# Kernel tuning notes

Measured on AMD Instinct MI355X. Metric: run time of the kernel, lower is better.

Reference implementation:

```python
import jax, jax.numpy as jnp
import numpy as np
import math

B, S, HID, NH, INTER, L = 8, 512, 768, 12, 3072, 4
DH = HID // NH
EPS = 1e-12


def setup_inputs() -> dict:
    key = jax.random.key(0)
    ks = jax.random.split(key, 12)
    s = 0.02
    hidden_states = jax.random.normal(ks[0], (B, S, HID), jnp.float32)
    lengths = jax.random.randint(ks[1], (B,), S // 2, S + 1)
    attention_mask = (jnp.arange(S)[None, :] < lengths[:, None]).astype(jnp.float32)
    return dict(
        hidden_states=hidden_states,
        attention_mask=attention_mask,
        Wqkv_w=jax.random.normal(ks[2], (L, 3 * HID, HID), jnp.float32) * s,
        Wqkv_b=jnp.zeros((L, 3 * HID), jnp.float32),
        attn_out_w=jax.random.normal(ks[3], (L, HID, HID), jnp.float32) * s,
        attn_out_b=jnp.zeros((L, HID), jnp.float32),
        ln1_g=jnp.ones((L, HID), jnp.float32),
        ln1_b=jnp.zeros((L, HID), jnp.float32),
        glu_w=jax.random.normal(ks[4], (L, 2 * INTER, HID), jnp.float32) * s,
        wo_w=jax.random.normal(ks[5], (L, HID, INTER), jnp.float32) * s,
        wo_b=jnp.zeros((L, HID), jnp.float32),
        ln2_g=jnp.ones((L, HID), jnp.float32),
        ln2_b=jnp.zeros((L, HID), jnp.float32),
        r1=1.0 + 0.1 * jax.random.normal(ks[6], (L, NH, 1, 1), jnp.float32),
        r2=1.0 + 0.1 * jax.random.normal(ks[7], (L, NH, 1, 1), jnp.float32),
        r3=1.0 + 0.1 * jax.random.normal(ks[8], (L, NH, 1, 1), jnp.float32),
    )


def _ln(x, g, b):
    mu = x.mean(-1, keepdims=True)
    var = ((x - mu) ** 2).mean(-1, keepdims=True)
    return (x - mu) / jnp.sqrt(var + EPS) * g + b


def _forward(hidden_states, attention_mask, Wqkv_w, Wqkv_b, attn_out_w, attn_out_b,
             ln1_g, ln1_b, glu_w, wo_w, wo_b, ln2_g, ln2_b, r1, r2, r3):
    mask = attention_mask  # [B,S] float, 1=valid
    pos = jnp.arange(S)
    rel = jnp.abs(pos[None, :] - pos[:, None]).astype(jnp.float32)  # [S,S]
    rel_pos = rel > 0
    attn_bias = (1.0 - mask)[:, None, None, :] * -10000.0  # [B,1,1,S]
    # unpad_input <-> zero invalid rows of padded tensor
    h = hidden_states * mask[:, :, None]
    for l in range(L):
        c1 = jnp.clip(r1[l], 1e-7)  # [NH,1,1]
        c2 = jnp.clip(r2[l], 1e-7)
        c3 = jnp.clip(r3[l], 1e-7)
        relp = jnp.where(rel_pos, rel, 1.0) ** c3  # [NH,S,S], safe pow at |i-j|=0
        relp = jnp.where(rel_pos, relp, 0.0)
        kb = -c1 * jnp.log1p(c2 * relp)  # kerple bias [NH,S,S]
        bias = attn_bias + kb[None]  # [B,NH,S,S]
        # qkv on valid tokens only (pad_input reinserts zeros)
        qkv = (h @ Wqkv_w[l].T + Wqkv_b[l]) * mask[:, :, None]
        qkv = qkv.reshape(B, S, 3, NH, DH)
        q = qkv[:, :, 0].transpose(0, 2, 1, 3)  # [B,NH,S,DH]
        k = qkv[:, :, 1].transpose(0, 2, 1, 3)
        v = qkv[:, :, 2].transpose(0, 2, 1, 3)
        scores = jnp.einsum('bhqd,bhkd->bhqk', q, k) / math.sqrt(DH) + bias
        probs = jax.nn.softmax(scores, axis=-1)
        attn = jnp.einsum('bhqk,bhkd->bhqd', probs, v)
        attn = attn.transpose(0, 2, 1, 3).reshape(B, S, HID)
        ao = _ln(attn @ attn_out_w[l].T + attn_out_b[l] + h, ln1_g[l], ln1_b[l])
        ao = ao * mask[:, :, None]
        g = ao @ glu_w[l].T  # [B,S,2*INTER]
        x = jax.nn.gelu(g[..., :INTER], approximate=False) * g[..., INTER:]
        h = _ln(x @ wo_w[l].T + wo_b[l] + ao, ln2_g[l], ln2_b[l])
        h = h * mask[:, :, None]
    return h


def reference(hidden_states, attention_mask, Wqkv_w, Wqkv_b, attn_out_w, attn_out_b,
              ln1_g, ln1_b, glu_w, wo_w, wo_b, ln2_g, ln2_b, r1, r2, r3):
    return _forward(hidden_states, attention_mask, Wqkv_w, Wqkv_b, attn_out_w,
                    attn_out_b, ln1_g, ln1_b, glu_w, wo_w, wo_b, ln2_g, ln2_b,
                    r1, r2, r3)
```

## Files before the change

### kernel.cpp

```cpp
#include <hip/hip_runtime.h>
#include <hip/hip_bf16.h>
#include <math.h>

#define BQ 8
#define SQ 512
#define HID 768
#define NH 12
#define DH 64
#define INTER 3072
#define NL 4
#define M_TOK (BQ*SQ)

typedef unsigned short ushort_t;
typedef __attribute__((ext_vector_type(8))) short bf16x8;
typedef __attribute__((ext_vector_type(8))) unsigned short u16x8;
typedef __attribute__((ext_vector_type(4))) float f32x4;

__device__ __forceinline__ float bf2f(ushort_t u) {
  union { float f; unsigned int i; } v; v.i = ((unsigned int)u) << 16; return v.f;
}
__device__ __forceinline__ ushort_t f2bf(float f) {
  __hip_bfloat16 h = __float2bfloat16(f);
  return *reinterpret_cast<ushort_t*>(&h);
}

__device__ __forceinline__ void gload_lds16(const ushort_t* g, ushort_t* l) {
  __builtin_amdgcn_global_load_lds(
      (const __attribute__((address_space(1))) void*)g,
      (__attribute__((address_space(3))) void*)l, 16, 0, 0);
}

template<int N>
__device__ __forceinline__ void wait_vm() {
  if constexpr (N == 0)      asm volatile("s_waitcnt vmcnt(0)" ::: "memory");
  else if constexpr (N == 6) asm volatile("s_waitcnt vmcnt(6)" ::: "memory");
  else if constexpr (N == 8) asm volatile("s_waitcnt vmcnt(8)" ::: "memory");
  else                       asm volatile("s_waitcnt vmcnt(12)" ::: "memory");
}

__global__ __launch_bounds__(256) void prep_kernel(
    const float* __restrict__ hidden, const float* __restrict__ amask,
    float* __restrict__ maskf, float* __restrict__ maskbias,
    float* __restrict__ h, ushort_t* __restrict__ hb)
{
  int i = blockIdx.x * 256 + threadIdx.x;
  if (i < M_TOK * HID) {
    float m = amask[i / HID];
    float v = hidden[i] * m;
    h[i] = v;
    hb[i] = f2bf(v);
    if (i < M_TOK) {
      maskf[i] = amask[i];
      maskbias[i] = (1.0f - amask[i]) * (-10000.0f);
    }
  }
}

__global__ void kerple_all_kernel(const float* __restrict__ r1,
                                  const float* __restrict__ r2,
                                  const float* __restrict__ r3,
                                  float* __restrict__ kbt_all)
{
  int lh = blockIdx.x;
  int d  = threadIdx.x;
  float c1 = fmaxf(r1[lh], 1e-7f);
  float c2 = fmaxf(r2[lh], 1e-7f);
  float c3 = fmaxf(r3[lh], 1e-7f);
  float v = 0.0f;
  if (d > 0) v = -c1 * log1pf(c2 * powf((float)d, c3));
  kbt_all[lh * SQ + d] = v;
}

#define WS0 (3*HID*HID)
#define WS1 (HID*HID)
#define WS2 (2*INTER*HID)
#define WS3 (HID*INTER)
#define WTOT (WS0+WS1+WS2+WS3)

__global__ __launch_bounds__(256) void wcast_layer_kernel(
    const float* __restrict__ w0, const float* __restrict__ w1,
    const float* __restrict__ w2, const float* __restrict__ w3,
    ushort_t* __restrict__ dst)
{
  int i = (blockIdx.x * 256 + threadIdx.x) * 4;
  if (i >= WTOT) return;
  const float* src; int off;
  if (i < WS0)                { src = w0; off = i; }
  else if (i < WS0+WS1)       { src = w1; off = i - WS0; }
  else if (i < WS0+WS1+WS2)   { src = w2; off = i - WS0 - WS1; }
  else                        { src = w3; off = i - WS0 - WS1 - WS2; }
  float4 v = *reinterpret_cast<const float4*>(src + off);
  ushort4 o;
  o.x = f2bf(v.x); o.y = f2bf(v.y); o.z = f2bf(v.z); o.w = f2bf(v.w);
  *reinterpret_cast<ushort4*>(dst + i) = o;
}

template<int MF, int NB, int BK, int EPI, int VN, int DB>
__global__ __launch_bounds__(256, 2) void mfma_gemm(
    const ushort_t* __restrict__ A, const ushort_t* __restrict__ B0p,
    const ushort_t* __restrict__ B1p, const float* __restrict__ bias,
    const float* __restrict__ rowscale, ushort_t* __restrict__ Cb,
    int N, int K)
{
  constexpr int BM   = MF * 32;
  constexpr int SMK  = BK / 8 - 1;
  constexpr int SSH  = (BK == 32) ? 1 : 0;
  constexpr int AIS  = (BM * BK * 2) / 4096;
  constexpr int BIS  = (128 * BK * 2) / 4096;
  constexpr int KH   = BK / 32;
  constexpr int NBUF = DB ? 2 : 1;

  __shared__ ushort_t As_[NBUF][BM * BK];
  __shared__ ushort_t Bs_[NBUF][NB][128 * BK];

  int tid = threadIdx.x;
  int lane = tid & 63, w = tid >> 6;
  int wr = w >> 1, wc = w & 1;
  int g = lane >> 4, r = lane & 15;

  int NBn = gridDim.x, NBm = gridDim.y;
  int lin = blockIdx.y * NBn + blockIdx.x;
  int cpx = (NBn * NBm) >> 3;
  int wg2 = (lin & 7) * cpx + (lin >> 3);
  int bn = wg2 / NBm, bm = wg2 % NBm;

  f32x4 acc[NB][MF][4];
#pragma unroll
  for (int p = 0; p < NB; ++p)
#pragma unroll
    for (int m = 0; m < MF; ++m)
#pragma unroll
      for (int n = 0; n < 4; ++n) acc[p][m][n] = (f32x4){0.f, 0.f, 0.f, 0.f};

  const ushort_t* Arow  = A   + (size_t)bm * BM * K;
  const ushort_t* Brow0 = B0p + (size_t)bn * 128 * K;
  const ushort_t* Brow1 = (NB == 2) ? (B1p + (size_t)bn * 128 * K) : nullptr;

  auto stage = [&](const ushort_t* base, ushort_t* lds, int k0, int ISS_w) {
#pragma unroll
    for (int i = 0; i < 4; ++i) {
      if (i >= ISS_w) break;
      int o   = (w * ISS_w + i) * 1024 + lane * 16;
      int row = o / (BK * 2);
      int pc  = (o >> 4) & SMK;
      int lc  = pc ^ ((row >> SSH) & SMK);
      gload_lds16(base + (size_t)row * K + k0 + lc * 8,
                  lds + ((w * ISS_w + i) << 9));
    }
  };
  auto stage_all = [&](int k0, int buf) {
    stage(Arow,  &As_[buf][0],    k0, AIS);
    stage(Brow0, &Bs_[buf][0][0], k0, BIS);
    if constexpr (NB == 2) stage(Brow1, &Bs_[buf][1][0], k0, BIS);
  };
  auto compute = [&](int buf) {
#pragma unroll
    for (int kh = 0; kh < KH; ++kh) {
      bf16x8 af[MF], bf_[4];
#pragma unroll
      for (int m = 0; m < MF; ++m)
        af[m] = *(const bf16x8*)(&As_[buf][(wr * (BM/2) + m * 16 + r) * BK
                  + (((kh * 4 + g) ^ ((r >> SSH) & SMK)) * 8)]);
#pragma unroll
      for (int n = 0; n < 4; ++n)
        bf_[n] = *(const bf16x8*)(&Bs_[buf][0][(wc * 64 + n * 16 + r) * BK
                  + (((kh * 4 + g) ^ ((r >> SSH) & SMK)) * 8)]);
#pragma unroll
      for (int m = 0; m < MF; ++m)
#pragma unroll
        for (int n = 0; n < 4; ++n)
          acc[0][m][n] = __builtin_amdgcn_mfma_f32_16x16x32_bf16(
              af[m], bf_[n], acc[0][m][n], 0, 0, 0);
      if constexpr (NB == 2) {
        bf16x8 bg[4];
#pragma unroll
        for (int n = 0; n < 4; ++n)
          bg[n] = *(const bf16x8*)(&Bs_[buf][1][(wc * 64 + n * 16 + r) * BK
                    + (((kh * 4 + g) ^ ((r >> SSH) & SMK)) * 8)]);
#pragma unroll
        for (int m = 0; m < MF; ++m)
#pragma unroll
          for (int n = 0; n < 4; ++n)
            acc[1][m][n] = __builtin_amdgcn_mfma_f32_16x16x32_bf16(
                af[m], bg[n], acc[1][m][n], 0, 0, 0);
      }
    }
  };

  int NT = K / BK;
  if constexpr (DB) {
    stage_all(0, 0);
    for (int t = 0; t < NT; ++t) {
      int cur = t & 1;
      if (t + 1 < NT) {
        stage_all((t + 1) * BK, cur ^ 1);
        wait_vm<VN>();
      } else {
        wait_vm<0>();
      }
      __builtin_amdgcn_s_barrier();
      compute(cur);
      __builtin_amdgcn_s_barrier();
    }
  } else {
    for (int t = 0; t < NT; ++t) {
      stage_all(t * BK, 0);
      wait_vm<0>();
      __builtin_amdgcn_s_barrier();
      compute(0);
      __builtin_amdgcn_s_barrier();
    }
  }

  int r0 = bm * BM + wr * (BM/2), c0 = bn * 128 + wc * 64;
#pragma unroll
  for (int m = 0; m < MF; ++m)
#pragma unroll
    for (int n = 0; n < 4; ++n) {
      int col  = c0 + n * 16 + (lane & 15);
      int rowb = r0 + m * 16 + (lane >> 4) * 4;
      if constexpr (EPI == 0) {
        float bv = bias ? bias[col] : 0.0f;
#pragma unroll
        for (int j = 0; j < 4; ++j)
          Cb[(size_t)(rowb + j) * N + col] = f2bf(acc[0][m][n][j] + bv);
      } else if constexpr (EPI == 1) {
#pragma unroll
        for (int j = 0; j < 4; ++j) {
          float va = acc[0][m][n][j];
          float vb = acc[1][m][n][j];
          float ge = 0.5f * va * (1.0f + erff(va * 0.70710678118654752440f));
          Cb[(size_t)(rowb + j) * N + col] = f2bf(ge * vb);
        }
      } else {
        float bv = bias ? bias[col] : 0.0f;
#pragma unroll
        for (int j = 0; j < 4; ++j) {
          float v = (acc[0][m][n][j] + bv) * rowscale[rowb + j];
          Cb[(size_t)(rowb + j) * N + col] = f2bf(v);
        }
      }
    }
}

__global__ __launch_bounds__(256) void attn_mfma(
    const ushort_t* __restrict__ qkvb, const float* __restrict__ kbt,
    const float* __restrict__ maskbias, ushort_t* __restrict__ attnb)
{
  __shared__ ushort_t Ks[64 * 64];
  __shared__ ushort_t Vt[64 * 64];
  __shared__ ushort_t Ps[64 * 64];
  __shared__ float    kbs[SQ];
  __shared__ float    mbs[SQ];

  int tid  = threadIdx.x;
  int lane = tid & 63, w = tid >> 6;
  int g = lane >> 4, r = lane & 15;
  int bid = blockIdx.x;
  int qt = (bid >> 3) & 7;
  int t_ = (bid & 7) * 12 + (bid >> 6);
  int hh = t_ % NH;
  int b  = t_ / NH;
  int q0 = qt * 64;

  for (int i = tid; i < SQ; i += 256) {
    kbs[i] = kbt[hh * SQ + i];
    mbs[i] = maskbias[b * SQ + i];
  }

  bf16x8 qf[2];
  {
    const ushort_t* qsrc = qkvb + (size_t)(b * SQ + q0 + w * 16 + r) * (3 * HID)
                         + hh * DH + g * 8;
    qf[0] = *(const bf16x8*)(qsrc);
    qf[1] = *(const bf16x8*)(qsrc + 32);
  }

  float m_run[4], l_run[4];
  f32x4 oacc[4];
#pragma unroll
  for (int j = 0; j < 4; ++j) { m_run[j] = -1e30f; l_run[j] = 0.f; }
#pragma unroll
  for (int nd = 0; nd < 4; ++nd) oacc[nd] = (f32x4){0.f, 0.f, 0.f, 0.f};

  int k2 = (tid & 31) * 2, dg = tid >> 5;

  for (int kc = 0; kc < 8; ++kc) {
    __syncthreads();
#pragma unroll
    for (int ii = 0; ii < 2; ++ii) {
      int row = (w * 2 + ii) * 8 + (lane >> 3);
      int c   = lane & 7;
      const ushort_t* src = qkvb + (size_t)(b * SQ + kc * 64 + row) * (3 * HID)
                          + HID + hh * DH + ((c ^ (row & 7)) * 8);
      gload_lds16(src, Ks + (w * 2 + ii) * 512 + lane * 8);
    }
    {
      const ushort_t* v0 = qkvb + (size_t)(b * SQ + kc * 64 + k2) * (3 * HID)
                         + 2 * HID + hh * DH + dg * 8;
      const ushort_t* v1 = v0 + 3 * HID;
      u16x8 a = *(const u16x8*)v0;
      u16x8 c = *(const u16x8*)v1;
#pragma unroll
      for (int u = 0; u < 8; ++u) {
        int d = dg * 8 + u;
        int addr = d * 64 + (((k2 >> 3) ^ (d & 7)) * 8) + (k2 & 7);
        ushort2 pr; pr.x = (ushort_t)a[u]; pr.y = (ushort_t)c[u];
        *(ushort2*)(Vt + addr) = pr;
      }
    }
    __syncthreads();

    f32x4 sacc[4];
#pragma unroll
    for (int n = 0; n < 4; ++n) sacc[n] = (f32x4){0.f, 0.f, 0.f, 0.f};
    __builtin_amdgcn_s_setprio(1);
#pragma unroll
    for (int kh = 0; kh < 2; ++kh) {
#pragma unroll
      for (int n = 0; n < 4; ++n) {
        bf16x8 kf = *(const bf16x8*)(Ks + (n * 16 + r) * 64
                                     + (((g + kh * 4) ^ (r & 7)) * 8));
        sacc[n] = __builtin_amdgcn_mfma_f32_16x16x32_bf16(qf[kh], kf, sacc[n], 0, 0, 0);
      }
    }
    __builtin_amdgcn_s_setprio(0);

    float sval[4][4], mx[4];
#pragma unroll
    for (int j = 0; j < 4; ++j) mx[j] = -1e30f;
#pragma unroll
    for (int n = 0; n < 4; ++n) {
      int kg = kc * 64 + n * 16 + r;
      float mb = mbs[kg];
#pragma unroll
      for (int j = 0; j < 4; ++j) {
        int qg = q0 + w * 16 + g * 4 + j;
        float s = sacc[n][j] * 0.125f + mb + kbs[abs(qg - kg)];
        sval[n][j] = s;
        mx[j] = fmaxf(mx[j], s);
      }
    }
#pragma unroll
    for (int j = 0; j < 4; ++j) {
      mx[j] = fmaxf(mx[j], __shfl_xor(mx[j], 1));
      mx[j] = fmaxf(mx[j], __shfl_xor(mx[j], 2));
      mx[j] = fmaxf(mx[j], __shfl_xor(mx[j], 4));
      mx[j] = fmaxf(mx[j], __shfl_xor(mx[j], 8));
      float mn = fmaxf(m_run[j], mx[j]);
      mx[j] = __expf(m_run[j] - mn);
      m_run[j] = mn;
    }
    float rs[4] = {0.f, 0.f, 0.f, 0.f};
#pragma unroll
    for (int n = 0; n < 4; ++n) {
#pragma unroll
      for (int j = 0; j < 4; ++j) {
        float pp = __expf(sval[n][j] - m_run[j]);
        int prow = w * 16 + g * 4 + j;
        int pcol = n * 16 + r;
        Ps[prow * 64 + (((pcol >> 3) ^ (prow & 7)) * 8) + (pcol & 7)] = f2bf(pp);
        rs[j] += pp;
      }
    }
#pragma unroll
    for (int j = 0; j < 4; ++j) {
      rs[j] += __shfl_xor(rs[j], 1);
      rs[j] += __shfl_xor(rs[j], 2);
      rs[j] += __shfl_xor(rs[j], 4);
      rs[j] += __shfl_xor(rs[j], 8);
      l_run[j] = l_run[j] * mx[j] + rs[j];
    }
#pragma unroll
    for (int nd = 0; nd < 4; ++nd)
#pragma unroll
      for (int j = 0; j < 4; ++j) oacc[nd][j] *= mx[j];

    __builtin_amdgcn_s_setprio(1);
#pragma unroll
    for (int kh = 0; kh < 2; ++kh) {
      bf16x8 pa = *(const bf16x8*)(Ps + (w * 16 + r) * 64
                                   + (((g + kh * 4) ^ (r & 7)) * 8));
#pragma unroll
      for (int nd = 0; nd < 4; ++nd) {
        bf16x8 vf = *(const bf16x8*)(Vt + (nd * 16 + r) * 64
                                     + (((g + kh * 4) ^ (r & 7)) * 8));
        oacc[nd] = __builtin_amdgcn_mfma_f32_16x16x32_bf16(pa, vf, oacc[nd], 0, 0, 0);
      }
    }
    __builtin_amdgcn_s_setprio(0);
  }

#pragma unroll
  for (int j = 0; j < 4; ++j) {
    float inv = 1.0f / l_run[j];
    int token = b * SQ + q0 + w * 16 + g * 4 + j;
#pragma unroll
    for (int nd = 0; nd < 4; ++nd)
      attnb[(size_t)token * HID + hh * DH + nd * 16 + r] = f2bf(oacc[nd][j] * inv);
  }
}

__global__ __launch_bounds__(256) void ln_res_kernel(
    const ushort_t* __restrict__ t, const float* __restrict__ res,
    const float* __restrict__ g, const float* __restrict__ bb,
    const float* __restrict__ maskf, float* __restrict__ out,
    ushort_t* __restrict__ outb)
{
  __shared__ float part[8];
  int row = blockIdx.x, tid = threadIdx.x;
  int wid = tid >> 6;
  const ushort_t* tp = t + (size_t)row * HID;
  const float*    rp = res + (size_t)row * HID;
  float y0 = bf2f(tp[tid      ]) + rp[tid      ];
  float y1 = bf2f(tp[tid + 256]) + rp[tid + 256];
  float y2 = bf2f(tp[tid + 512]) + rp[tid + 512];

  float s = y0 + y1 + y2;
  s += __shfl_xor(s, 1);  s += __shfl_xor(s, 2);  s += __shfl_xor(s, 4);
  s += __shfl_xor(s, 8);  s += __shfl_xor(s, 16); s += __shfl_xor(s, 32);
  if ((tid & 63) == 0) part[wid] = s;
  __syncthreads();
  float mu = (part[0] + part[1] + part[2] + part[3]) * (1.0f / 768.0f);

  float d0 = y0 - mu, d1 = y1 - mu, d2 = y2 - mu;
  float v = d0*d0 + d1*d1 + d2*d2;
  v += __shfl_xor(v, 1);  v += __shfl_xor(v, 2);  v += __shfl_xor(v, 4);
  v += __shfl_xor(v, 8);  v += __shfl_xor(v, 16); v += __shfl_xor(v, 32);
  if ((tid & 63) == 0) part[4 + wid] = v;
  __syncthreads();
  float rstd = rsqrtf((part[4] + part[5] + part[6] + part[7]) * (1.0f / 768.0f)
                      + 1e-12f);
  float mk = maskf[row];
  float v0 = (d0*rstd*g[tid      ] + bb[tid      ]) * mk;
  float v1 = (d1*rstd*g[tid + 256] + bb[tid + 256]) * mk;
  float v2 = (d2*rstd*g[tid + 512] + bb[tid + 512]) * mk;
  size_t base = (size_t)row * HID;
  out[base + tid      ] = v0;  outb[base + tid      ] = f2bf(v0);
  out[base + tid + 256] = v1;  outb[base + tid + 256] = f2bf(v1);
  out[base + tid + 512] = v2;  outb[base + tid + 512] = f2bf(v2);
}

extern "C" void kernel_launch(void* const* d_in, const int* in_sizes, int n_in,
                              void* d_out, int out_size, void* d_ws, size_t ws_size,
                              hipStream_t stream) {
  const float* hidden     = (const float*)d_in[0];
  const float* amask      = (const float*)d_in[1];
  const float* Wqkv_w     = (const float*)d_in[2];
  const float* Wqkv_b     = (const float*)d_in[3];
  const float* attn_out_w = (const float*)d_in[4];
  const float* attn_out_b = (const float*)d_in[5];
  const float* ln1_g      = (const float*)d_in[6];
  const float* ln1_b      = (const float*)d_in[7];
  const float* glu_w      = (const float*)d_in[8];
  const float* wo_w       = (const float*)d_in[9];
  const float* wo_b       = (const float*)d_in[10];
  const float* ln2_g      = (const float*)d_in[11];
  const float* ln2_b      = (const float*)d_in[12];
  const float* r1         = (const float*)d_in[13];
  const float* r2         = (const float*)d_in[14];
  const float* r3         = (const float*)d_in[15];

  float* ws       = (float*)d_ws;
  float* maskf    = ws;
  float* maskbias = maskf    + 4096;
  float* kbt_all  = maskbias + 4096;
  float* h        = kbt_all  + NL*NH*SQ;
  float* ao       = h  + (size_t)M_TOK*HID;
  ushort_t* us    = (ushort_t*)(ao + (size_t)M_TOK*HID);
  ushort_t* hb    = us;
  ushort_t* aob   = hb    + (size_t)M_TOK*HID;
  ushort_t* atnb  = aob   + (size_t)M_TOK*HID;
  ushort_t* tb    = atnb  + (size_t)M_TOK*HID;
  ushort_t* qkv_b = tb    + (size_t)M_TOK*HID;
  ushort_t* xb    = qkv_b + (size_t)M_TOK*3*HID;
  ushort_t* wbf   = xb    + (size_t)M_TOK*INTER;

  prep_kernel<<<(M_TOK*HID + 255)/256, 256, 0, stream>>>(
      hidden, amask, maskf, maskbias, h, hb);
  kerple_all_kernel<<<NL*NH, SQ, 0, stream>>>(r1, r2, r3, kbt_all);

  for (int l = 0; l < NL; ++l) {
    wcast_layer_kernel<<<(WTOT/4 + 255)/256, 256, 0, stream>>>(
        Wqkv_w     + (size_t)l*WS0,
        attn_out_w + (size_t)l*WS1,
        glu_w      + (size_t)l*WS2,
        wo_w       + (size_t)l*WS3, wbf);
    ushort_t* wqkv = wbf;
    ushort_t* wao  = wbf + WS0;
    ushort_t* wga  = wbf + WS0 + WS1;
    ushort_t* wgb  = wga + (size_t)INTER*HID;
    ushort_t* wwo  = wbf + WS0 + WS1 + WS2;

    mfma_gemm<4,1,64,2,8,1><<<dim3(3*HID/128, M_TOK/128), 256, 0, stream>>>(
        hb, wqkv, nullptr, Wqkv_b + (size_t)l*3*HID, maskf, qkv_b, 3*HID, HID);

    attn_mfma<<<BQ*NH*8, 256, 0, stream>>>(
        qkv_b, kbt_all + (size_t)l*NH*SQ, maskbias, atnb);

    mfma_gemm<2,1,64,0,6,1><<<dim3(HID/128, M_TOK/64), 256, 0, stream>>>(
        atnb, wao, nullptr, attn_out_b + (size_t)l*HID, nullptr, tb, HID, HID);

    ln_res_kernel<<<M_TOK, 256, 0, stream>>>(tb, h, ln1_g + (size_t)l*HID,
                                             ln1_b + (size_t)l*HID, maskf, ao, aob);

    mfma_gemm<4,2,64,1,0,0><<<dim3(INTER/128, M_TOK/128), 256, 0, stream>>>(
        aob, wga, wgb, nullptr, nullptr, xb, INTER, HID);

    mfma_gemm<2,1,64,0,6,1><<<dim3(HID/128, M_TOK/64), 256, 0, stream>>>(
        xb, wwo, nullptr, wo_b + (size_t)l*HID, nullptr, tb, HID, INTER);

    float* hout = (l == NL - 1) ? (float*)d_out : h;
    ln_res_kernel<<<M_TOK, 256, 0, stream>>>(tb, ao, ln2_g + (size_t)l*HID,
                                             ln2_b + (size_t)l*HID, maskf, hout, hb);
  }
}
```

Before: 829.3 us.

## Keep residual stream in bf16 only and drop GEMM tile swizzle

Removes the fp32 copies of the residual stream (h, ao). The layernorm-residual kernels now read the bf16 residual and write fp32 output only for the final layer, which cuts global memory traffic in the prep and layernorm kernels. It also replaces the grouped block-index remapping in the GEMM with plain blockIdx mapping, which may change L2 reuse. The cost is lower residual precision, since errors from bf16 rounding can accumulate across the layers.

```diff
diff --git a/kernel.cpp b/kernel.cpp
--- a/kernel.cpp
+++ b/kernel.cpp
@@ -41,14 +41,12 @@
 __global__ __launch_bounds__(256) void prep_kernel(
     const float* __restrict__ hidden, const float* __restrict__ amask,
     float* __restrict__ maskf, float* __restrict__ maskbias,
-    float* __restrict__ h, ushort_t* __restrict__ hb)
+    ushort_t* __restrict__ hb)
 {
   int i = blockIdx.x * 256 + threadIdx.x;
   if (i < M_TOK * HID) {
     float m = amask[i / HID];
-    float v = hidden[i] * m;
-    h[i] = v;
-    hb[i] = f2bf(v);
+    hb[i] = f2bf(hidden[i] * m);
     if (i < M_TOK) {
       maskf[i] = amask[i];
       maskbias[i] = (1.0f - amask[i]) * (-10000.0f);
@@ -117,12 +115,7 @@
   int lane = tid & 63, w = tid >> 6;
   int wr = w >> 1, wc = w & 1;
   int g = lane >> 4, r = lane & 15;
-
-  int NBn = gridDim.x, NBm = gridDim.y;
-  int lin = blockIdx.y * NBn + blockIdx.x;
-  int cpx = (NBn * NBm) >> 3;
-  int wg2 = (lin & 7) * cpx + (lin >> 3);
-  int bn = wg2 / NBm, bm = wg2 % NBm;
+  int bn = blockIdx.x, bm = blockIdx.y;
 
   f32x4 acc[NB][MF][4];
 #pragma unroll
@@ -402,19 +395,19 @@
 }
 
 __global__ __launch_bounds__(256) void ln_res_kernel(
-    const ushort_t* __restrict__ t, const float* __restrict__ res,
+    const ushort_t* __restrict__ t, const ushort_t* __restrict__ res,
     const float* __restrict__ g, const float* __restrict__ bb,
-    const float* __restrict__ maskf, float* __restrict__ out,
+    const float* __restrict__ maskf, float* __restrict__ outf,
     ushort_t* __restrict__ outb)
 {
   __shared__ float part[8];
   int row = blockIdx.x, tid = threadIdx.x;
   int wid = tid >> 6;
-  const ushort_t* tp = t + (size_t)row * HID;
-  const float*    rp = res + (size_t)row * HID;
-  float y0 = bf2f(tp[tid      ]) + rp[tid      ];
-  float y1 = bf2f(tp[tid + 256]) + rp[tid + 256];
-  float y2 = bf2f(tp[tid + 512]) + rp[tid + 512];
+  const ushort_t* tp = t   + (size_t)row * HID;
+  const ushort_t* rp = res + (size_t)row * HID;
+  float y0 = bf2f(tp[tid      ]) + bf2f(rp[tid      ]);
+  float y1 = bf2f(tp[tid + 256]) + bf2f(rp[tid + 256]);
+  float y2 = bf2f(tp[tid + 512]) + bf2f(rp[tid + 512]);
 
   float s = y0 + y1 + y2;
   s += __shfl_xor(s, 1);  s += __shfl_xor(s, 2);  s += __shfl_xor(s, 4);
@@ -436,9 +429,14 @@
   float v1 = (d1*rstd*g[tid + 256] + bb[tid + 256]) * mk;
   float v2 = (d2*rstd*g[tid + 512] + bb[tid + 512]) * mk;
   size_t base = (size_t)row * HID;
-  out[base + tid      ] = v0;  outb[base + tid      ] = f2bf(v0);
-  out[base + tid + 256] = v1;  outb[base + tid + 256] = f2bf(v1);
-  out[base + tid + 512] = v2;  outb[base + tid + 512] = f2bf(v2);
+  outb[base + tid      ] = f2bf(v0);
+  outb[base + tid + 256] = f2bf(v1);
+  outb[base + tid + 512] = f2bf(v2);
+  if (outf) {
+    outf[base + tid      ] = v0;
+    outf[base + tid + 256] = v1;
+    outf[base + tid + 512] = v2;
+  }
 }
 
 extern "C" void kernel_launch(void* const* d_in, const int* in_sizes, int n_in,
@@ -465,9 +463,7 @@
   float* maskf    = ws;
   float* maskbias = maskf    + 4096;
   float* kbt_all  = maskbias + 4096;
-  float* h        = kbt_all  + NL*NH*SQ;
-  float* ao       = h  + (size_t)M_TOK*HID;
-  ushort_t* us    = (ushort_t*)(ao + (size_t)M_TOK*HID);
+  ushort_t* us    = (ushort_t*)(kbt_all + NL*NH*SQ);
   ushort_t* hb    = us;
   ushort_t* aob   = hb    + (size_t)M_TOK*HID;
   ushort_t* atnb  = aob   + (size_t)M_TOK*HID;
@@ -477,7 +473,7 @@
   ushort_t* wbf   = xb    + (size_t)M_TOK*INTER;
 
   prep_kernel<<<(M_TOK*HID + 255)/256, 256, 0, stream>>>(
-      hidden, amask, maskf, maskbias, h, hb);
+      hidden, amask, maskf, maskbias, hb);
   kerple_all_kernel<<<NL*NH, SQ, 0, stream>>>(r1, r2, r3, kbt_all);
 
   for (int l = 0; l < NL; ++l) {
@@ -501,8 +497,9 @@
     mfma_gemm<2,1,64,0,6,1><<<dim3(HID/128, M_TOK/64), 256, 0, stream>>>(
         atnb, wao, nullptr, attn_out_b + (size_t)l*HID, nullptr, tb, HID, HID);
 
-    ln_res_kernel<<<M_TOK, 256, 0, stream>>>(tb, h, ln1_g + (size_t)l*HID,
-                                             ln1_b + (size_t)l*HID, maskf, ao, aob);
+    ln_res_kernel<<<M_TOK, 256, 0, stream>>>(tb, hb, ln1_g + (size_t)l*HID,
+                                             ln1_b + (size_t)l*HID, maskf,
+                                             nullptr, aob);
 
     mfma_gemm<4,2,64,1,0,0><<<dim3(INTER/128, M_TOK/128), 256, 0, stream>>>(
         aob, wga, wgb, nullptr, nullptr, xb, INTER, HID);
@@ -510,8 +507,9 @@
     mfma_gemm<2,1,64,0,6,1><<<dim3(HID/128, M_TOK/64), 256, 0, stream>>>(
         xb, wwo, nullptr, wo_b + (size_t)l*HID, nullptr, tb, HID, INTER);
 
-    float* hout = (l == NL - 1) ? (float*)d_out : h;
-    ln_res_kernel<<<M_TOK, 256, 0, stream>>>(tb, ao, ln2_g + (size_t)l*HID,
-                                             ln2_b + (size_t)l*HID, maskf, hout, hb);
-  }
-}
+    float* hout = (l == NL - 1) ? (float*)d_out : nullptr;
+    ln_res_kernel<<<M_TOK, 256, 0, stream>>>(tb, aob, ln2_g + (size_t)l*HID,
+                                             ln2_b + (size_t)l*HID, maskf,
+                                             hout, hb);
+  }
+}
```

Result: faster. 778.5 us (-6.1%).
